# Kernel tuning notes

Hardware: AMD Instinct MI355X
Metric: run time of the kernel (lower is better)

The kernel has to match this reference:

```python
import jax, jax.numpy as jnp
import numpy as np

T = 8388608  # sequence length (2^23)
WIDTH = 1.0


def phi(x, width=WIDTH):
    # Phi(x) = x if x > 0; x + width if x < -width; 0 otherwise
    return jnp.maximum(x, 0.0) + jnp.minimum(x + width, 0.0)


def setup_inputs() -> dict:
    key = jax.random.key(0)
    k1, k2 = jax.random.split(key)
    inputs = jax.random.normal(k1, (1, T), dtype=jnp.float32)
    state = jnp.zeros((1, 1), dtype=jnp.float32)
    # non_neg constrained scalar weight
    kernel = jax.random.uniform(k2, (1, 1), dtype=jnp.float32)
    return {"inputs": inputs, "state": state, "kernel": kernel}


def reference(inputs, state, kernel):
    # outputs_ = inputs * kernel (scalar multiply), then sequential hysteresis scan:
    #   out_i = Phi(outputs_[i] - out_{i-1}) + out_{i-1}
    xs = (inputs * kernel[0, 0])[0]  # [T]

    def step(prev, x):
        out = phi(x - prev) + prev
        return out, out

    last, outs = jax.lax.scan(step, state[0, 0], xs)
    outputs = outs.reshape(inputs.shape)       # [1, T]
    new_state = last.reshape(1, 1)             # [1, 1]
    return outputs, new_state
```

## Files before the change

kernel.cpp:

```cpp
#include <hip/hip_runtime.h>
#include <math.h>


#define TPB 256
#define WAVES (TPB / 64)
#define SEGS 4
#define FPL 8
#define SEG_ELEMS (TPB * FPL)
#define ELEMS (SEGS * SEG_ELEMS)

typedef float v4f __attribute__((ext_vector_type(4)));

__device__ __forceinline__ float clampf(float x, float lo, float hi) {
    return fminf(fmaxf(x, lo), hi);
}

__global__ __launch_bounds__(TPB) void k_agg(const v4f* __restrict__ x4,
                                             const float* __restrict__ kern,
                                             float2* __restrict__ agg) {
    __shared__ float wl[SEGS][WAVES], wh[SEGS][WAVES];
    const int t = threadIdx.x, lane = t & 63, w = t >> 6;
    const int b = blockIdx.x;
    const float k = kern[0];
    const size_t base4 = (size_t)b * (ELEMS / 4);

    v4f v[SEGS][2];
#pragma unroll
    for (int s = 0; s < SEGS; ++s) {
        const size_t i4 = base4 + (size_t)s * (SEG_ELEMS / 4) + (size_t)t * 2;
        v[s][0] = x4[i4];
        v[s][1] = x4[i4 + 1];
    }

#pragma unroll
    for (int s = 0; s < SEGS; ++s) {
        float lo, hi, a;
        a = v[s][0].x * k; lo = a; hi = a + 1.0f;
        a = v[s][0].y * k; lo = clampf(lo, a, a + 1.0f); hi = clampf(hi, a, a + 1.0f);
        a = v[s][0].z * k; lo = clampf(lo, a, a + 1.0f); hi = clampf(hi, a, a + 1.0f);
        a = v[s][0].w * k; lo = clampf(lo, a, a + 1.0f); hi = clampf(hi, a, a + 1.0f);
        a = v[s][1].x * k; lo = clampf(lo, a, a + 1.0f); hi = clampf(hi, a, a + 1.0f);
        a = v[s][1].y * k; lo = clampf(lo, a, a + 1.0f); hi = clampf(hi, a, a + 1.0f);
        a = v[s][1].z * k; lo = clampf(lo, a, a + 1.0f); hi = clampf(hi, a, a + 1.0f);
        a = v[s][1].w * k; lo = clampf(lo, a, a + 1.0f); hi = clampf(hi, a, a + 1.0f);
#pragma unroll
        for (int off = 1; off < 64; off <<= 1) {
            float plo = __shfl_down(lo, off);
            float phi_ = __shfl_down(hi, off);
            float nlo = clampf(lo, plo, phi_);
            float nhi = clampf(hi, plo, phi_);
            lo = nlo; hi = nhi;
        }
        if (lane == 0) { wl[s][w] = lo; wh[s][w] = hi; }
    }
    __syncthreads();
    if (t == 0) {
        float L = -INFINITY, H = INFINITY;
#pragma unroll
        for (int s = 0; s < SEGS; ++s)
#pragma unroll
            for (int i = 0; i < WAVES; ++i) {
                L = clampf(L, wl[s][i], wh[s][i]);
                H = clampf(H, wl[s][i], wh[s][i]);
            }
        agg[b] = make_float2(L, H);
    }
}

__global__ __launch_bounds__(TPB) void k_apply(
    const v4f* __restrict__ x4,
    const float* __restrict__ kern,
    const float* __restrict__ state,
    const float2* __restrict__ agg,
    float* __restrict__ out,
    int nblocks)
{
    __shared__ float rl[WAVES], rh[WAVES];
    __shared__ float wtl[SEGS][WAVES], wth[SEGS][WAVES];
    __shared__ float s_vb;

    const int t = threadIdx.x, lane = t & 63, w = t >> 6;
    const int b = blockIdx.x;
    const float k = kern[0];
    const size_t base4 = (size_t)b * (ELEMS / 4);

    v4f v[SEGS][2];
#pragma unroll
    for (int s = 0; s < SEGS; ++s) {
        const size_t i4 = base4 + (size_t)s * (SEG_ELEMS / 4) + (size_t)t * 2;
        v[s][0] = __builtin_nontemporal_load(&x4[i4]);
        v[s][1] = __builtin_nontemporal_load(&x4[i4 + 1]);
    }

    {
        const int per = nblocks / TPB;
        float lo = -INFINITY, hi = INFINITY;
#pragma unroll
        for (int c = 0; c < per; ++c) {
            int j = t * per + c;
            if (j < b) {
                float2 ag = agg[j];
                lo = clampf(lo, ag.x, ag.y);
                hi = clampf(hi, ag.x, ag.y);
            }
        }
#pragma unroll
        for (int off = 1; off < 64; off <<= 1) {
            float plo = __shfl_down(lo, off);
            float phi_ = __shfl_down(hi, off);
            float nlo = clampf(lo, plo, phi_);
            float nhi = clampf(hi, plo, phi_);
            lo = nlo; hi = nhi;
        }
        if (lane == 0) { rl[w] = lo; rh[w] = hi; }
    }
    __syncthreads();
    if (t == 0) {
        float L = rl[0], H = rh[0];
#pragma unroll
        for (int i = 1; i < WAVES; ++i) {
            L = clampf(L, rl[i], rh[i]);
            H = clampf(H, rl[i], rh[i]);
        }
        s_vb = clampf(state[0], L, H);
    }

    float a[SEGS][FPL];
    float eslo[SEGS], eshi[SEGS];
    float Slo[SEGS], Shi[SEGS];

#pragma unroll
    for (int s = 0; s < SEGS; ++s) {
        a[s][0] = v[s][0].x * k; a[s][1] = v[s][0].y * k;
        a[s][2] = v[s][0].z * k; a[s][3] = v[s][0].w * k;
        a[s][4] = v[s][1].x * k; a[s][5] = v[s][1].y * k;
        a[s][6] = v[s][1].z * k; a[s][7] = v[s][1].w * k;
        float lo = a[s][0], hi = a[s][0] + 1.0f;
#pragma unroll
        for (int c = 1; c < FPL; ++c) {
            lo = clampf(lo, a[s][c], a[s][c] + 1.0f);
            hi = clampf(hi, a[s][c], a[s][c] + 1.0f);
        }
#pragma unroll
        for (int off = 1; off < 64; off <<= 1) {
            float plo = __shfl_up(lo, off);
            float phi_ = __shfl_up(hi, off);
            if (lane >= off) {
                float nlo = clampf(plo, lo, hi);
                float nhi = clampf(phi_, lo, hi);
                lo = nlo; hi = nhi;
            }
        }
        float elo = __shfl_up(lo, 1), ehi = __shfl_up(hi, 1);
        if (lane == 0) { elo = -INFINITY; ehi = INFINITY; }
        eslo[s] = elo; eshi[s] = ehi;
        if (lane == 63) { wtl[s][w] = lo; wth[s][w] = hi; }
    }
    __syncthreads();

#pragma unroll
    for (int s = 0; s < SEGS; ++s) {
        float welo = -INFINITY, wehi = INFINITY;
        for (int i = 0; i < w; ++i) {
            welo = clampf(welo, wtl[s][i], wth[s][i]);
            wehi = clampf(wehi, wtl[s][i], wth[s][i]);
        }
        float llo = eslo[s], lhi = eshi[s];
        eslo[s] = clampf(welo, llo, lhi);
        eshi[s] = clampf(wehi, llo, lhi);
        float stl = -INFINITY, sth = INFINITY;
#pragma unroll
        for (int i = 0; i < WAVES; ++i) {
            stl = clampf(stl, wtl[s][i], wth[s][i]);
            sth = clampf(sth, wtl[s][i], wth[s][i]);
        }
        Slo[s] = stl; Shi[s] = sth;
    }

    __syncthreads();
    float p = s_vb;
    float wv = p;
#pragma unroll
    for (int s = 0; s < SEGS; ++s) {
        wv = clampf(p, eslo[s], eshi[s]);
        v4f r0, r1;
        wv = clampf(wv, a[s][0], a[s][0] + 1.0f); r0.x = wv;
        wv = clampf(wv, a[s][1], a[s][1] + 1.0f); r0.y = wv;
        wv = clampf(wv, a[s][2], a[s][2] + 1.0f); r0.z = wv;
        wv = clampf(wv, a[s][3], a[s][3] + 1.0f); r0.w = wv;
        wv = clampf(wv, a[s][4], a[s][4] + 1.0f); r1.x = wv;
        wv = clampf(wv, a[s][5], a[s][5] + 1.0f); r1.y = wv;
        wv = clampf(wv, a[s][6], a[s][6] + 1.0f); r1.z = wv;
        wv = clampf(wv, a[s][7], a[s][7] + 1.0f); r1.w = wv;
        v4f* o = (v4f*)(out + (size_t)b * ELEMS + (size_t)s * SEG_ELEMS) + (size_t)t * 2;
        __builtin_nontemporal_store(r0, &o[0]);
        __builtin_nontemporal_store(r1, &o[1]);
        p = clampf(p, Slo[s], Shi[s]);
    }

    if (b == nblocks - 1 && t == TPB - 1)
        out[(size_t)nblocks * ELEMS] = wv;
}

extern "C" void kernel_launch(void* const* d_in, const int* in_sizes, int n_in,
                              void* d_out, int out_size, void* d_ws, size_t ws_size,
                              hipStream_t stream) {
    const v4f* x4      = (const v4f*)d_in[0];
    const float* state = (const float*)d_in[1];
    const float* kern  = (const float*)d_in[2];
    float* out = (float*)d_out;

    const size_t T = (size_t)in_sizes[0];
    const int nblocks = (int)(T / ELEMS);
    float2* agg = (float2*)d_ws;

    k_agg<<<nblocks, TPB, 0, stream>>>(x4, kern, agg);
    k_apply<<<nblocks, TPB, 0, stream>>>(x4, kern, state, agg, out, nblocks);
}
```

Baseline: 100.6 us.

## Fuse aggregate and apply kernels into one pass with an atomic grid barrier

Merges the two-kernel decoupled scan into a single kernel. Each of 256 blocks covers four chunks, publishes its clamp-interval aggregate through a release store and an atomic counter, then spins until every block has arrived. After that it computes its exclusive prefix with one agg load per thread and re-reads the input to emit outputs. This removes a kernel launch and the separate prefix loop over the aggregates. The cost is a memset launch, far fewer resident waves per CU for latency hiding, and a spin barrier that relies on all blocks being co-resident.

```diff
diff --git a/kernel.cpp b/kernel.cpp
--- a/kernel.cpp
+++ b/kernel.cpp
@@ -1,48 +1,113 @@
 #include <hip/hip_runtime.h>
 #include <math.h>
+#include <stdint.h>
 
 
 #define TPB 256
-#define WAVES (TPB / 64)
+#define WAVES 4
 #define SEGS 4
 #define FPL 8
 #define SEG_ELEMS (TPB * FPL)
-#define ELEMS (SEGS * SEG_ELEMS)
+#define CHUNK_ELEMS (SEGS * SEG_ELEMS)
+#define CHUNKS 4
+#define BLK_ELEMS (CHUNKS * CHUNK_ELEMS)
 
 typedef float v4f __attribute__((ext_vector_type(4)));
 
 __device__ __forceinline__ float clampf(float x, float lo, float hi) {
     return fminf(fmaxf(x, lo), hi);
 }
-
-__global__ __launch_bounds__(TPB) void k_agg(const v4f* __restrict__ x4,
-                                             const float* __restrict__ kern,
-                                             float2* __restrict__ agg) {
+__device__ __forceinline__ uint64_t pack2(float lo, float hi) {
+    union { float f[2]; uint64_t u; } u; u.f[0] = lo; u.f[1] = hi; return u.u;
+}
+__device__ __forceinline__ void unpack2(uint64_t w, float* lo, float* hi) {
+    union { uint64_t u; float f[2]; } u; u.u = w; *lo = u.f[0]; *hi = u.f[1];
+}
+
+__global__ __launch_bounds__(TPB) void phi_scan(
+    const v4f* __restrict__ x4,
+    const float* __restrict__ kern,
+    const float* __restrict__ state,
+    float* __restrict__ out,
+    uint64_t* __restrict__ agg,
+    uint32_t* __restrict__ counter,
+    int nblocks)
+{
     __shared__ float wl[SEGS][WAVES], wh[SEGS][WAVES];
+    __shared__ float rl[WAVES], rh[WAVES];
+    __shared__ float s_v;
+
     const int t = threadIdx.x, lane = t & 63, w = t >> 6;
     const int b = blockIdx.x;
     const float k = kern[0];
-    const size_t base4 = (size_t)b * (ELEMS / 4);
-
-    v4f v[SEGS][2];
-#pragma unroll
-    for (int s = 0; s < SEGS; ++s) {
-        const size_t i4 = base4 + (size_t)s * (SEG_ELEMS / 4) + (size_t)t * 2;
-        v[s][0] = x4[i4];
-        v[s][1] = x4[i4 + 1];
-    }
-
-#pragma unroll
-    for (int s = 0; s < SEGS; ++s) {
-        float lo, hi, a;
-        a = v[s][0].x * k; lo = a; hi = a + 1.0f;
-        a = v[s][0].y * k; lo = clampf(lo, a, a + 1.0f); hi = clampf(hi, a, a + 1.0f);
-        a = v[s][0].z * k; lo = clampf(lo, a, a + 1.0f); hi = clampf(hi, a, a + 1.0f);
-        a = v[s][0].w * k; lo = clampf(lo, a, a + 1.0f); hi = clampf(hi, a, a + 1.0f);
-        a = v[s][1].x * k; lo = clampf(lo, a, a + 1.0f); hi = clampf(hi, a, a + 1.0f);
-        a = v[s][1].y * k; lo = clampf(lo, a, a + 1.0f); hi = clampf(hi, a, a + 1.0f);
-        a = v[s][1].z * k; lo = clampf(lo, a, a + 1.0f); hi = clampf(hi, a, a + 1.0f);
-        a = v[s][1].w * k; lo = clampf(lo, a, a + 1.0f); hi = clampf(hi, a, a + 1.0f);
+    const size_t blk4 = (size_t)b * (BLK_ELEMS / 4);
+
+    float bLo = -INFINITY, bHi = INFINITY;
+    for (int c = 0; c < CHUNKS; ++c) {
+        const size_t c4 = blk4 + (size_t)c * (CHUNK_ELEMS / 4);
+        v4f v[SEGS][2];
+#pragma unroll
+        for (int s = 0; s < SEGS; ++s) {
+            const size_t i4 = c4 + (size_t)s * (SEG_ELEMS / 4) + (size_t)t * 2;
+            v[s][0] = x4[i4];
+            v[s][1] = x4[i4 + 1];
+        }
+#pragma unroll
+        for (int s = 0; s < SEGS; ++s) {
+            float lo, hi, a;
+            a = v[s][0].x * k; lo = a; hi = a + 1.0f;
+            a = v[s][0].y * k; lo = clampf(lo, a, a + 1.0f); hi = clampf(hi, a, a + 1.0f);
+            a = v[s][0].z * k; lo = clampf(lo, a, a + 1.0f); hi = clampf(hi, a, a + 1.0f);
+            a = v[s][0].w * k; lo = clampf(lo, a, a + 1.0f); hi = clampf(hi, a, a + 1.0f);
+            a = v[s][1].x * k; lo = clampf(lo, a, a + 1.0f); hi = clampf(hi, a, a + 1.0f);
+            a = v[s][1].y * k; lo = clampf(lo, a, a + 1.0f); hi = clampf(hi, a, a + 1.0f);
+            a = v[s][1].z * k; lo = clampf(lo, a, a + 1.0f); hi = clampf(hi, a, a + 1.0f);
+            a = v[s][1].w * k; lo = clampf(lo, a, a + 1.0f); hi = clampf(hi, a, a + 1.0f);
+#pragma unroll
+            for (int off = 1; off < 64; off <<= 1) {
+                float plo = __shfl_down(lo, off);
+                float phi_ = __shfl_down(hi, off);
+                float nlo = clampf(lo, plo, phi_);
+                float nhi = clampf(hi, plo, phi_);
+                lo = nlo; hi = nhi;
+            }
+            if (lane == 0) { wl[s][w] = lo; wh[s][w] = hi; }
+        }
+        __syncthreads();
+        if (t == 0) {
+#pragma unroll
+            for (int s = 0; s < SEGS; ++s)
+#pragma unroll
+                for (int i = 0; i < WAVES; ++i) {
+                    bLo = clampf(bLo, wl[s][i], wh[s][i]);
+                    bHi = clampf(bHi, wl[s][i], wh[s][i]);
+                }
+        }
+        __syncthreads();
+    }
+
+    if (t == 0) {
+        __hip_atomic_store(&agg[b], pack2(bLo, bHi),
+                           __ATOMIC_RELEASE, __HIP_MEMORY_SCOPE_AGENT);
+        __hip_atomic_fetch_add(counter, 1u,
+                               __ATOMIC_RELEASE, __HIP_MEMORY_SCOPE_AGENT);
+    }
+    __syncthreads();
+    if (t == 0) {
+        while (__hip_atomic_load(counter, __ATOMIC_ACQUIRE,
+                                 __HIP_MEMORY_SCOPE_AGENT) < (uint32_t)nblocks)
+            __builtin_amdgcn_s_sleep(16);
+    }
+    __syncthreads();
+
+    {
+        float lo = -INFINITY, hi = INFINITY;
+        if (t < b) {
+            float l, h;
+            unpack2(__hip_atomic_load(&agg[t], __ATOMIC_RELAXED,
+                                      __HIP_MEMORY_SCOPE_AGENT), &l, &h);
+            lo = l; hi = h;
+        }
 #pragma unroll
         for (int off = 1; off < 64; off <<= 1) {
             float plo = __shfl_down(lo, off);
@@ -51,155 +116,95 @@
             float nhi = clampf(hi, plo, phi_);
             lo = nlo; hi = nhi;
         }
-        if (lane == 0) { wl[s][w] = lo; wh[s][w] = hi; }
-    }
-    __syncthreads();
-    if (t == 0) {
-        float L = -INFINITY, H = INFINITY;
-#pragma unroll
-        for (int s = 0; s < SEGS; ++s)
+        if (lane == 0) { rl[w] = lo; rh[w] = hi; }
+        __syncthreads();
+        if (t == 0) {
+            float L = rl[0], H = rh[0];
+#pragma unroll
+            for (int i = 1; i < WAVES; ++i) {
+                L = clampf(L, rl[i], rh[i]);
+                H = clampf(H, rl[i], rh[i]);
+            }
+            s_v = clampf(state[0], L, H);
+        }
+        __syncthreads();
+    }
+
+    float p = s_v;
+    for (int c = 0; c < CHUNKS; ++c) {
+        const size_t c4 = blk4 + (size_t)c * (CHUNK_ELEMS / 4);
+        float a[SEGS][FPL];
+        float eslo[SEGS], eshi[SEGS], Slo[SEGS], Shi[SEGS];
+#pragma unroll
+        for (int s = 0; s < SEGS; ++s) {
+            const size_t i4 = c4 + (size_t)s * (SEG_ELEMS / 4) + (size_t)t * 2;
+            v4f v0 = __builtin_nontemporal_load(&x4[i4]);
+            v4f v1 = __builtin_nontemporal_load(&x4[i4 + 1]);
+            a[s][0] = v0.x * k; a[s][1] = v0.y * k; a[s][2] = v0.z * k; a[s][3] = v0.w * k;
+            a[s][4] = v1.x * k; a[s][5] = v1.y * k; a[s][6] = v1.z * k; a[s][7] = v1.w * k;
+            float lo = a[s][0], hi = a[s][0] + 1.0f;
+#pragma unroll
+            for (int j = 1; j < FPL; ++j) {
+                lo = clampf(lo, a[s][j], a[s][j] + 1.0f);
+                hi = clampf(hi, a[s][j], a[s][j] + 1.0f);
+            }
+#pragma unroll
+            for (int off = 1; off < 64; off <<= 1) {
+                float plo = __shfl_up(lo, off);
+                float phi_ = __shfl_up(hi, off);
+                if (lane >= off) {
+                    float nlo = clampf(plo, lo, hi);
+                    float nhi = clampf(phi_, lo, hi);
+                    lo = nlo; hi = nhi;
+                }
+            }
+            float elo = __shfl_up(lo, 1), ehi = __shfl_up(hi, 1);
+            if (lane == 0) { elo = -INFINITY; ehi = INFINITY; }
+            eslo[s] = elo; eshi[s] = ehi;
+            if (lane == 63) { wl[s][w] = lo; wh[s][w] = hi; }
+        }
+        __syncthreads();
+#pragma unroll
+        for (int s = 0; s < SEGS; ++s) {
+            float welo = -INFINITY, wehi = INFINITY;
+            for (int i = 0; i < w; ++i) {
+                welo = clampf(welo, wl[s][i], wh[s][i]);
+                wehi = clampf(wehi, wl[s][i], wh[s][i]);
+            }
+            float llo = eslo[s], lhi = eshi[s];
+            eslo[s] = clampf(welo, llo, lhi);
+            eshi[s] = clampf(wehi, llo, lhi);
+            float stl = -INFINITY, sth = INFINITY;
 #pragma unroll
             for (int i = 0; i < WAVES; ++i) {
-                L = clampf(L, wl[s][i], wh[s][i]);
-                H = clampf(H, wl[s][i], wh[s][i]);
-            }
-        agg[b] = make_float2(L, H);
-    }
-}
-
-__global__ __launch_bounds__(TPB) void k_apply(
-    const v4f* __restrict__ x4,
-    const float* __restrict__ kern,
-    const float* __restrict__ state,
-    const float2* __restrict__ agg,
-    float* __restrict__ out,
-    int nblocks)
-{
-    __shared__ float rl[WAVES], rh[WAVES];
-    __shared__ float wtl[SEGS][WAVES], wth[SEGS][WAVES];
-    __shared__ float s_vb;
-
-    const int t = threadIdx.x, lane = t & 63, w = t >> 6;
-    const int b = blockIdx.x;
-    const float k = kern[0];
-    const size_t base4 = (size_t)b * (ELEMS / 4);
-
-    v4f v[SEGS][2];
-#pragma unroll
-    for (int s = 0; s < SEGS; ++s) {
-        const size_t i4 = base4 + (size_t)s * (SEG_ELEMS / 4) + (size_t)t * 2;
-        v[s][0] = __builtin_nontemporal_load(&x4[i4]);
-        v[s][1] = __builtin_nontemporal_load(&x4[i4 + 1]);
-    }
-
-    {
-        const int per = nblocks / TPB;
-        float lo = -INFINITY, hi = INFINITY;
-#pragma unroll
-        for (int c = 0; c < per; ++c) {
-            int j = t * per + c;
-            if (j < b) {
-                float2 ag = agg[j];
-                lo = clampf(lo, ag.x, ag.y);
-                hi = clampf(hi, ag.x, ag.y);
-            }
-        }
-#pragma unroll
-        for (int off = 1; off < 64; off <<= 1) {
-            float plo = __shfl_down(lo, off);
-            float phi_ = __shfl_down(hi, off);
-            float nlo = clampf(lo, plo, phi_);
-            float nhi = clampf(hi, plo, phi_);
-            lo = nlo; hi = nhi;
-        }
-        if (lane == 0) { rl[w] = lo; rh[w] = hi; }
-    }
-    __syncthreads();
-    if (t == 0) {
-        float L = rl[0], H = rh[0];
-#pragma unroll
-        for (int i = 1; i < WAVES; ++i) {
-            L = clampf(L, rl[i], rh[i]);
-            H = clampf(H, rl[i], rh[i]);
-        }
-        s_vb = clampf(state[0], L, H);
-    }
-
-    float a[SEGS][FPL];
-    float eslo[SEGS], eshi[SEGS];
-    float Slo[SEGS], Shi[SEGS];
-
-#pragma unroll
-    for (int s = 0; s < SEGS; ++s) {
-        a[s][0] = v[s][0].x * k; a[s][1] = v[s][0].y * k;
-        a[s][2] = v[s][0].z * k; a[s][3] = v[s][0].w * k;
-        a[s][4] = v[s][1].x * k; a[s][5] = v[s][1].y * k;
-        a[s][6] = v[s][1].z * k; a[s][7] = v[s][1].w * k;
-        float lo = a[s][0], hi = a[s][0] + 1.0f;
-#pragma unroll
-        for (int c = 1; c < FPL; ++c) {
-            lo = clampf(lo, a[s][c], a[s][c] + 1.0f);
-            hi = clampf(hi, a[s][c], a[s][c] + 1.0f);
-        }
-#pragma unroll
-        for (int off = 1; off < 64; off <<= 1) {
-            float plo = __shfl_up(lo, off);
-            float phi_ = __shfl_up(hi, off);
-            if (lane >= off) {
-                float nlo = clampf(plo, lo, hi);
-                float nhi = clampf(phi_, lo, hi);
-                lo = nlo; hi = nhi;
-            }
-        }
-        float elo = __shfl_up(lo, 1), ehi = __shfl_up(hi, 1);
-        if (lane == 0) { elo = -INFINITY; ehi = INFINITY; }
-        eslo[s] = elo; eshi[s] = ehi;
-        if (lane == 63) { wtl[s][w] = lo; wth[s][w] = hi; }
-    }
-    __syncthreads();
-
-#pragma unroll
-    for (int s = 0; s < SEGS; ++s) {
-        float welo = -INFINITY, wehi = INFINITY;
-        for (int i = 0; i < w; ++i) {
-            welo = clampf(welo, wtl[s][i], wth[s][i]);
-            wehi = clampf(wehi, wtl[s][i], wth[s][i]);
-        }
-        float llo = eslo[s], lhi = eshi[s];
-        eslo[s] = clampf(welo, llo, lhi);
-        eshi[s] = clampf(wehi, llo, lhi);
-        float stl = -INFINITY, sth = INFINITY;
-#pragma unroll
-        for (int i = 0; i < WAVES; ++i) {
-            stl = clampf(stl, wtl[s][i], wth[s][i]);
-            sth = clampf(sth, wtl[s][i], wth[s][i]);
-        }
-        Slo[s] = stl; Shi[s] = sth;
-    }
-
-    __syncthreads();
-    float p = s_vb;
-    float wv = p;
-#pragma unroll
-    for (int s = 0; s < SEGS; ++s) {
-        wv = clampf(p, eslo[s], eshi[s]);
-        v4f r0, r1;
-        wv = clampf(wv, a[s][0], a[s][0] + 1.0f); r0.x = wv;
-        wv = clampf(wv, a[s][1], a[s][1] + 1.0f); r0.y = wv;
-        wv = clampf(wv, a[s][2], a[s][2] + 1.0f); r0.z = wv;
-        wv = clampf(wv, a[s][3], a[s][3] + 1.0f); r0.w = wv;
-        wv = clampf(wv, a[s][4], a[s][4] + 1.0f); r1.x = wv;
-        wv = clampf(wv, a[s][5], a[s][5] + 1.0f); r1.y = wv;
-        wv = clampf(wv, a[s][6], a[s][6] + 1.0f); r1.z = wv;
-        wv = clampf(wv, a[s][7], a[s][7] + 1.0f); r1.w = wv;
-        v4f* o = (v4f*)(out + (size_t)b * ELEMS + (size_t)s * SEG_ELEMS) + (size_t)t * 2;
-        __builtin_nontemporal_store(r0, &o[0]);
-        __builtin_nontemporal_store(r1, &o[1]);
-        p = clampf(p, Slo[s], Shi[s]);
-    }
-
-    if (b == nblocks - 1 && t == TPB - 1)
-        out[(size_t)nblocks * ELEMS] = wv;
+                stl = clampf(stl, wl[s][i], wh[s][i]);
+                sth = clampf(sth, wl[s][i], wh[s][i]);
+            }
+            Slo[s] = stl; Shi[s] = sth;
+        }
+#pragma unroll
+        for (int s = 0; s < SEGS; ++s) {
+            float wv = clampf(p, eslo[s], eshi[s]);
+            v4f r0, r1;
+            wv = clampf(wv, a[s][0], a[s][0] + 1.0f); r0.x = wv;
+            wv = clampf(wv, a[s][1], a[s][1] + 1.0f); r0.y = wv;
+            wv = clampf(wv, a[s][2], a[s][2] + 1.0f); r0.z = wv;
+            wv = clampf(wv, a[s][3], a[s][3] + 1.0f); r0.w = wv;
+            wv = clampf(wv, a[s][4], a[s][4] + 1.0f); r1.x = wv;
+            wv = clampf(wv, a[s][5], a[s][5] + 1.0f); r1.y = wv;
+            wv = clampf(wv, a[s][6], a[s][6] + 1.0f); r1.z = wv;
+            wv = clampf(wv, a[s][7], a[s][7] + 1.0f); r1.w = wv;
+            v4f* o = (v4f*)(out + (size_t)b * BLK_ELEMS + (size_t)c * CHUNK_ELEMS
+                            + (size_t)s * SEG_ELEMS) + (size_t)t * 2;
+            __builtin_nontemporal_store(r0, &o[0]);
+            __builtin_nontemporal_store(r1, &o[1]);
+            p = clampf(p, Slo[s], Shi[s]);
+        }
+        __syncthreads();
+    }
+
+    if (b == nblocks - 1 && t == 0)
+        out[(size_t)nblocks * BLK_ELEMS] = p;
 }
 
 extern "C" void kernel_launch(void* const* d_in, const int* in_sizes, int n_in,
@@ -211,9 +216,12 @@
     float* out = (float*)d_out;
 
     const size_t T = (size_t)in_sizes[0];
-    const int nblocks = (int)(T / ELEMS);
-    float2* agg = (float2*)d_ws;
-
-    k_agg<<<nblocks, TPB, 0, stream>>>(x4, kern, agg);
-    k_apply<<<nblocks, TPB, 0, stream>>>(x4, kern, state, agg, out, nblocks);
-}
+    const int nblocks = (int)(T / BLK_ELEMS);
+
+    uint32_t* counter = (uint32_t*)d_ws;
+    uint64_t* agg = (uint64_t*)((char*)d_ws + 16);
+
+    hipMemsetAsync(d_ws, 0, 16, stream);
+    phi_scan<<<nblocks, TPB, 0, stream>>>(x4, kern, state, out,
+                                          agg, counter, nblocks);
+}
```

Result: slower. 118.0 us (+17.3%).
